# Optimization experiments

Measured on AMD Instinct MI355X. Metric: run time of the kernel, lower is better.

## Reference

```python
import jax, jax.numpy as jnp
import numpy as np

E = 8           # experts (num_experts // world_size, world_size=1)
D = 1024        # hidden_size
H = 4096        # expert FFN hidden = 4*D
CAP_FACTOR = 1.25
LOSS_COEF = 0.01


def setup_inputs() -> dict:
    key = jax.random.key(0)
    k0, k1, k2, k3 = jax.random.split(key, 4)
    B, N = 8, 2048
    x = jax.random.normal(k0, (B, N, D), jnp.float32)
    Wg = jax.random.normal(k1, (D, E), jnp.float32) * (D ** -0.5)
    W1 = jax.random.normal(k2, (E, D, H), jnp.float32) * (D ** -0.5)
    b1 = jnp.zeros((E, H), jnp.float32)
    W2 = jax.random.normal(k3, (E, H, D), jnp.float32) * (H ** -0.5)
    b2 = jnp.zeros((E, D), jnp.float32)
    return {"hidden_states": x, "Wg": Wg, "W1": W1, "b1": b1, "W2": W2, "b2": b2}


def reference(hidden_states, Wg, W1, b1, W2, b2):
    x = hidden_states
    B, N, Dm = x.shape
    S = B * N
    C = int(S * CAP_FACTOR / E)      # shared expert capacity (top1+top2)
    xt = x.reshape(S, Dm)

    # --- top-2 gating ---
    gates = jax.nn.softmax(xt @ Wg, axis=-1)                       # [S, E]
    idx1 = jnp.argmax(gates, axis=-1)                              # [S]
    gate1 = jnp.take_along_axis(gates, idx1[:, None], axis=-1)[:, 0]
    gates_m = gates.at[jnp.arange(S), idx1].set(-1.0)
    idx2 = jnp.argmax(gates_m, axis=-1)
    gate2 = jnp.take_along_axis(gates, idx2[:, None], axis=-1)[:, 0]

    mask1 = jax.nn.one_hot(idx1, E, dtype=xt.dtype)                # [S, E]
    mask2 = jax.nn.one_hot(idx2, E, dtype=xt.dtype)

    # positions within each expert's buffer (top-1 first, then top-2)
    pos1 = jnp.take_along_axis(jnp.cumsum(mask1, axis=0), idx1[:, None], axis=1)[:, 0] - 1.0
    keep1 = (pos1 < C).astype(xt.dtype)
    used1 = jnp.sum(mask1 * keep1[:, None], axis=0)                # [E] slots taken by top-1
    pos2 = jnp.take_along_axis(jnp.cumsum(mask2, axis=0), idx2[:, None], axis=1)[:, 0] - 1.0
    pos2 = pos2 + used1[idx2]
    keep2 = (pos2 < C).astype(xt.dtype)

    # renormalize surviving gates
    denom = gate1 * keep1 + gate2 * keep2 + 1e-9
    g1 = gate1 * keep1 / denom
    g2 = gate2 * keep2 / denom

    p1 = jnp.where(keep1 > 0, pos1, 0.0).astype(jnp.int32)
    p2 = jnp.where(keep2 > 0, pos2, 0.0).astype(jnp.int32)

    # --- dispatch (scatter tokens into [E, C, D] expert buffers) ---
    buf = jnp.zeros((E, C, Dm), xt.dtype)
    buf = buf.at[idx1, p1].add(xt * keep1[:, None])
    buf = buf.at[idx2, p2].add(xt * keep2[:, None])

    # --- expert grouped FFN ---
    h = jax.nn.gelu(jnp.einsum('ecd,edh->ech', buf, W1) + b1[:, None, :])
    eo = jnp.einsum('ech,ehd->ecd', h, W2) + b2[:, None, :]       # [E, C, D]

    # --- combine (gather + weight) ---
    y = g1[:, None] * eo[idx1, p1] + g2[:, None] * eo[idx2, p2]    # [S, D]

    # --- load-balancing aux loss ---
    me = jnp.mean(gates, axis=0)        # density proxy
    ce = jnp.mean(mask1, axis=0)        # actual top-1 density
    loss = LOSS_COEF * jnp.mean(me * ce) * (E * E)

    # output dropout is identity in eval / deterministic mode
    return y.reshape(B, N, Dm), loss
```

## Files before the change

kernel.cpp:

```cpp
#include <hip/hip_runtime.h>
#include <hip/hip_bf16.h>

#define S_TOKENS 16384
#define DMODEL   1024
#define NEXP     8
#define HFF      4096
#define CAP      2560
#define OUT_TOTAL (S_TOKENS * DMODEL + 1)
#define NCHUNK   64

typedef __attribute__((ext_vector_type(8))) short bf16x8;
typedef __attribute__((ext_vector_type(4))) float f32x4;

__device__ inline float bf2f(unsigned short u) {
    union { unsigned int i; float f; } v; v.i = ((unsigned int)u) << 16; return v.f;
}
__device__ inline unsigned short f2bf(float f) {
    __hip_bfloat16 h = __float2bfloat16(f);
    return *reinterpret_cast<unsigned short*>(&h);
}
__device__ inline float ldg(const void* p, size_t i, int f32i) {
    return f32i ? ((const float*)p)[i] : bf2f(((const ushort*)p)[i]);
}
__device__ inline float gelu_tanh(float x) {
    float u = 0.7978845608028654f * (x + 0.044715f * x * x * x);
    return 0.5f * x * (1.0f + tanhf(u));
}
__device__ inline void lds16(const void* g, void* l) {
    __builtin_amdgcn_global_load_lds((const __attribute__((address_space(1))) unsigned int*)g,
                                     (__attribute__((address_space(3))) unsigned int*)l, 16, 0, 0);
}

__global__ void detect_kernel(const ushort* __restrict__ xus, int* __restrict__ flag) {
    const int lane = threadIdx.x;
    int cnt = 0;
#pragma unroll
    for (int j = 0; j < 16; j++) {
        int p = lane * 16 + j;
        int eb = (xus[2 * p] >> 7) & 0xFF;
        cnt += (eb >= 100 && eb <= 140) ? 1 : 0;
    }
#pragma unroll
    for (int off = 32; off > 0; off >>= 1) cnt += __shfl_down(cnt, off, 64);
    if (lane == 0) flag[0] = (cnt < 512) ? 1 : 0;
}

__global__ __launch_bounds__(256) void zero_kernel(void* __restrict__ out, const int* __restrict__ dflag) {
    const int f32i = *dflag;
    for (size_t i = (size_t)blockIdx.x * 256 + threadIdx.x; i < OUT_TOTAL; i += (size_t)gridDim.x * 256) {
        if (f32i) ((float*)out)[i] = 0.f; else ((ushort*)out)[i] = 0;
    }
}

__global__ __launch_bounds__(256) void zeroeo_kernel(float* __restrict__ p, size_t n) {
    for (size_t i = (size_t)blockIdx.x * 256 + threadIdx.x; i < n; i += (size_t)gridDim.x * 256)
        p[i] = 0.f;
}

__global__ __launch_bounds__(256) void convx_kernel(const void* __restrict__ x, const int* __restrict__ dflag,
                                                    ushort* __restrict__ xb) {
    const int f32i = *dflag;
    for (size_t i = (size_t)blockIdx.x * 256 + threadIdx.x; i < (size_t)S_TOKENS * DMODEL;
         i += (size_t)gridDim.x * 256)
        xb[i] = f32i ? f2bf(((const float*)x)[i]) : ((const ushort*)x)[i];
}

__global__ __launch_bounds__(256) void gate_kernel(const void* __restrict__ x, const void* __restrict__ Wg,
                                                   const int* __restrict__ dflag,
                                                   float* __restrict__ gate1, float* __restrict__ gate2,
                                                   int* __restrict__ idx1, int* __restrict__ idx2,
                                                   float* __restrict__ bsum) {
    __shared__ float wgs[DMODEL * NEXP];
    __shared__ float gsh[4][NEXP];
    const int t = threadIdx.x;
    const int f32i = *dflag;
    for (int i = t; i < DMODEL * NEXP; i += 256) wgs[i] = ldg(Wg, i, f32i);
    __syncthreads();
    const int wave = t >> 6, lane = t & 63;
    const int s = blockIdx.x * 4 + wave;
    float acc[NEXP];
#pragma unroll
    for (int e = 0; e < NEXP; e++) acc[e] = 0.f;
#pragma unroll
    for (int i = 0; i < 16; i++) {
        int d = i * 64 + lane;
        float xv = ldg(x, (size_t)s * DMODEL + d, f32i);
        const float* w = &wgs[d * NEXP];
#pragma unroll
        for (int e = 0; e < NEXP; e++) acc[e] += xv * w[e];
    }
#pragma unroll
    for (int off = 32; off > 0; off >>= 1)
#pragma unroll
        for (int e = 0; e < NEXP; e++) acc[e] += __shfl_down(acc[e], off, 64);
    if (lane == 0) {
        float mx = acc[0];
#pragma unroll
        for (int e = 1; e < NEXP; e++) mx = fmaxf(mx, acc[e]);
        float p[NEXP], se = 0.f;
#pragma unroll
        for (int e = 0; e < NEXP; e++) { p[e] = __expf(acc[e] - mx); se += p[e]; }
        float inv = 1.0f / se;
#pragma unroll
        for (int e = 0; e < NEXP; e++) p[e] *= inv;
        int i1 = 0; float g1v = p[0];
#pragma unroll
        for (int e = 1; e < NEXP; e++) if (p[e] > g1v) { g1v = p[e]; i1 = e; }
        int i2 = -1; float g2v = -1.0f;
#pragma unroll
        for (int e = 0; e < NEXP; e++) if (e != i1 && p[e] > g2v) { g2v = p[e]; i2 = e; }
        gate1[s] = g1v; gate2[s] = g2v; idx1[s] = i1; idx2[s] = i2;
#pragma unroll
        for (int e = 0; e < NEXP; e++) gsh[wave][e] = p[e];
    }
    __syncthreads();
    if (t < NEXP) bsum[blockIdx.x * NEXP + t] = gsh[0][t] + gsh[1][t] + gsh[2][t] + gsh[3][t];
}

__global__ __launch_bounds__(256) void hist_kernel(const int* __restrict__ idx1, const int* __restrict__ idx2,
                                                   const float* __restrict__ bsum,
                                                   int* __restrict__ c1, int* __restrict__ c2,
                                                   float* __restrict__ msumB, int* __restrict__ rowmap) {
    const int b = blockIdx.x, t = threadIdx.x;
    const int w = t >> 6, lane = t & 63;
    __shared__ int sc1[4][NEXP], sc2[4][NEXP];
    __shared__ float sm[256];

    for (int i = b * 256 + t; i < NEXP * CAP; i += NCHUNK * 256) rowmap[i] = -1;

    const int s = b * 256 + w * 64 + lane;
    const int id1 = idx1[s], id2 = idx2[s];
#pragma unroll
    for (int e = 0; e < NEXP; e++) {
        unsigned long long m1 = __ballot(id1 == e);
        unsigned long long m2 = __ballot(id2 == e);
        if (lane == 0) { sc1[w][e] = __popcll(m1); sc2[w][e] = __popcll(m2); }
    }
    sm[t] = bsum[b * 512 + t] + bsum[b * 512 + 256 + t];
    __syncthreads();
    if (t < NEXP) {
        c1[b * NEXP + t] = sc1[0][t] + sc1[1][t] + sc1[2][t] + sc1[3][t];
        c2[b * NEXP + t] = sc2[0][t] + sc2[1][t] + sc2[2][t] + sc2[3][t];
        float ms = 0.f;
#pragma unroll
        for (int k = 0; k < 32; k++) ms += sm[t + NEXP * k];
        msumB[b * NEXP + t] = ms;
    }
}

__global__ void base_kernel(const int* __restrict__ c1, const int* __restrict__ c2,
                            const float* __restrict__ msumB, const int* __restrict__ dflag,
                            int* __restrict__ base1, int* __restrict__ base2, void* __restrict__ out) {
    const int lane = threadIdx.x;
    float contrib = 0.f;
    if (lane < NEXP) {
        int run = 0;
        for (int b = 0; b < NCHUNK; b++) { base1[b * NEXP + lane] = run; run += c1[b * NEXP + lane]; }
        const int count1 = run;
        int run2 = count1 < CAP ? count1 : CAP;
        for (int b = 0; b < NCHUNK; b++) { base2[b * NEXP + lane] = run2; run2 += c2[b * NEXP + lane]; }
        float ms = 0.f;
        for (int b = 0; b < NCHUNK; b++) ms += msumB[b * NEXP + lane];
        contrib = (ms / (float)S_TOKENS) * ((float)count1 / (float)S_TOKENS);
    }
#pragma unroll
    for (int off = 4; off > 0; off >>= 1) contrib += __shfl_down(contrib, off, 64);
    if (lane == 0) {
        float L = 0.08f * contrib;
        if (*dflag) ((float*)out)[(size_t)S_TOKENS * DMODEL] = L;
        else        ((ushort*)out)[(size_t)S_TOKENS * DMODEL] = f2bf(L);
    }
}

__global__ __launch_bounds__(256) void place_kernel(const int* __restrict__ idx1, const int* __restrict__ idx2,
                                                    const int* __restrict__ base1, const int* __restrict__ base2,
                                                    int* __restrict__ p1i, int* __restrict__ p2i,
                                                    int* __restrict__ rowmap) {
    const int b = blockIdx.x, t = threadIdx.x;
    const int w = t >> 6, lane = t & 63;
    const unsigned long long below = (1ull << lane) - 1ull;
    __shared__ int wc1[4][NEXP], wc2[4][NEXP];
    const int s = b * 256 + w * 64 + lane;
    const int id1 = idx1[s], id2 = idx2[s];
    int r1 = 0, r2 = 0;
#pragma unroll
    for (int e = 0; e < NEXP; e++) {
        unsigned long long m1 = __ballot(id1 == e);
        if (id1 == e) r1 = __popcll(m1 & below);
        unsigned long long m2 = __ballot(id2 == e);
        if (id2 == e) r2 = __popcll(m2 & below);
        if (lane == 0) { wc1[w][e] = __popcll(m1); wc2[w][e] = __popcll(m2); }
    }
    __syncthreads();
    int off1 = 0, off2 = 0;
#pragma unroll
    for (int ww = 0; ww < 3; ww++) {
        if (ww < w) { off1 += wc1[ww][id1]; off2 += wc2[ww][id2]; }
    }
    const int pos1 = base1[b * NEXP + id1] + off1 + r1;
    if (pos1 < CAP) { p1i[s] = pos1; rowmap[id1 * CAP + pos1] = s; } else p1i[s] = -1;
    const int pos2 = base2[b * NEXP + id2] + off2 + r2;
    if (pos2 < CAP) { p2i[s] = pos2; rowmap[id2 * CAP + pos2] = s; } else p2i[s] = -1;
}

__global__ __launch_bounds__(256) void transpose_conv(const void* __restrict__ src, ushort* __restrict__ dst,
                                                      const int* __restrict__ dflag,
                                                      long srcBase, int srcStride, int dstStride,
                                                      long srcExpStride, long dstExpStride) {
    __shared__ ushort tile[64][68];
    const int f32i = *dflag;
    srcBase += (long)blockIdx.z * srcExpStride;
    dst     += (size_t)blockIdx.z * dstExpStride;
    const int c0 = blockIdx.x * 64, r0 = blockIdx.y * 64;
    const int tx = threadIdx.x & 15, ty = threadIdx.x >> 4;
#pragma unroll
    for (int k = 0; k < 4; k++) {
        int row = ty + 16 * k;
        size_t b = (size_t)srcBase + (size_t)(r0 + row) * srcStride + c0 + tx * 4;
#pragma unroll
        for (int j = 0; j < 4; j++) tile[row][tx * 4 + j] = f2bf(ldg(src, b + j, f32i));
    }
    __syncthreads();
#pragma unroll
    for (int k = 0; k < 4; k++) {
        int orow = ty + 16 * k;
        ushort4 v;
        v.x = tile[tx * 4 + 0][orow];
        v.y = tile[tx * 4 + 1][orow];
        v.z = tile[tx * 4 + 2][orow];
        v.w = tile[tx * 4 + 3][orow];
        *(ushort4*)(dst + (size_t)(c0 + orow) * dstStride + r0 + tx * 4) = v;
    }
}

template<int NC>
__global__ __launch_bounds__(256) void gemm1_kernel(const ushort* __restrict__ xb,
                                                    const int* __restrict__ rowmapBase,
                                                    const ushort* __restrict__ T,
                                                    const void* __restrict__ b1, long biasBase,
                                                    const int* __restrict__ dflag,
                                                    ushort* __restrict__ hout) {
    __shared__ ushort lA[128 * 32];
    __shared__ ushort lB[128 * 32];
    const int z = blockIdx.z;
    const int* rowmapE = rowmapBase + z * CAP;
    T    += (size_t)z * NC * DMODEL;
    hout += (size_t)z * CAP * NC;
    biasBase += (long)z * HFF;
    const int t = threadIdx.x;
    const int w = t >> 6, lane = t & 63;
    const int n0 = blockIdx.x * 128, m0 = blockIdx.y * 128;
    const int wr = w >> 1, wc = w & 1;
    const int l15 = lane & 15, quad = lane >> 4;
    const int swz = (lane >> 3) & 3;
    const int q2 = quad ^ ((l15 >> 1) & 3);

    int arow[2];
#pragma unroll
    for (int it = 0; it < 2; it++) {
        int r = (it * 2048 + w * 512 + lane * 8) >> 5;
        int rm = rowmapE[m0 + r];
        arow[it] = rm < 0 ? 0 : rm;
    }

    f32x4 acc[4][4];
#pragma unroll
    for (int i = 0; i < 4; i++)
#pragma unroll
        for (int j = 0; j < 4; j++) acc[i][j] = (f32x4){0.f, 0.f, 0.f, 0.f};

    for (int k0 = 0; k0 < DMODEL; k0 += 32) {
        __syncthreads();
#pragma unroll
        for (int it = 0; it < 2; it++) {
            int f = it * 2048 + w * 512 + lane * 8;
            int r = f >> 5, kk = (f & 31) ^ (swz << 3);
            lds16(xb + (size_t)arow[it] * DMODEL + k0 + kk, &lA[it * 2048 + w * 512]);
            lds16(T + (size_t)(n0 + r) * DMODEL + k0 + kk, &lB[it * 2048 + w * 512]);
        }
        __syncthreads();
        bf16x8 af[4], bfr[4];
#pragma unroll
        for (int i = 0; i < 4; i++) af[i] = *(const bf16x8*)&lA[(wr * 64 + i * 16 + l15) * 32 + q2 * 8];
#pragma unroll
        for (int j = 0; j < 4; j++) bfr[j] = *(const bf16x8*)&lB[(wc * 64 + j * 16 + l15) * 32 + q2 * 8];
#pragma unroll
        for (int i = 0; i < 4; i++)
#pragma unroll
            for (int j = 0; j < 4; j++)
                acc[i][j] = __builtin_amdgcn_mfma_f32_16x16x32_bf16(af[i], bfr[j], acc[i][j], 0, 0, 0);
    }
    const int f32i = *dflag;
    float bv[4];
#pragma unroll
    for (int j = 0; j < 4; j++) bv[j] = ldg(b1, biasBase + n0 + wc * 64 + j * 16 + l15, f32i);
#pragma unroll
    for (int i = 0; i < 4; i++) {
        int row0 = m0 + wr * 64 + i * 16 + quad * 4;
#pragma unroll
        for (int j = 0; j < 4; j++) {
            int col = n0 + wc * 64 + j * 16 + l15;
#pragma unroll
            for (int r = 0; r < 4; r++)
                hout[(size_t)(row0 + r) * NC + col] = f2bf(gelu_tanh(acc[i][j][r] + bv[j]));
        }
    }
}

template<int KC>
__global__ __launch_bounds__(256) void gemm2f_kernel(const ushort* __restrict__ h,
                                                     const ushort* __restrict__ T2,
                                                     float* __restrict__ eo32) {
    __shared__ ushort lA[128 * 32];
    __shared__ ushort lB[128 * 32];
    const int ze = blockIdx.z;
    h    += (size_t)ze * CAP * KC;
    T2   += (size_t)ze * DMODEL * KC;
    eo32 += (size_t)ze * CAP * DMODEL;
    const int t = threadIdx.x;
    const int w = t >> 6, lane = t & 63;
    const int n0 = blockIdx.x * 128, m0 = blockIdx.y * 128;
    const int wr = w >> 1, wc = w & 1;
    const int l15 = lane & 15, quad = lane >> 4;
    const int swz = (lane >> 3) & 3;
    const int q2 = quad ^ ((l15 >> 1) & 3);

    f32x4 acc[4][4];
#pragma unroll
    for (int i = 0; i < 4; i++)
#pragma unroll
        for (int j = 0; j < 4; j++) acc[i][j] = (f32x4){0.f, 0.f, 0.f, 0.f};

    for (int k0 = 0; k0 < KC; k0 += 32) {
        __syncthreads();
#pragma unroll
        for (int it = 0; it < 2; it++) {
            int f = it * 2048 + w * 512 + lane * 8;
            int r = f >> 5, kk = (f & 31) ^ (swz << 3);
            lds16(h  + (size_t)(m0 + r) * KC + k0 + kk, &lA[it * 2048 + w * 512]);
            lds16(T2 + (size_t)(n0 + r) * KC + k0 + kk, &lB[it * 2048 + w * 512]);
        }
        __syncthreads();
        bf16x8 af[4], bfr[4];
#pragma unroll
        for (int i = 0; i < 4; i++) af[i] = *(const bf16x8*)&lA[(wr * 64 + i * 16 + l15) * 32 + q2 * 8];
#pragma unroll
        for (int j = 0; j < 4; j++) bfr[j] = *(const bf16x8*)&lB[(wc * 64 + j * 16 + l15) * 32 + q2 * 8];
#pragma unroll
        for (int i = 0; i < 4; i++)
#pragma unroll
            for (int j = 0; j < 4; j++)
                acc[i][j] = __builtin_amdgcn_mfma_f32_16x16x32_bf16(af[i], bfr[j], acc[i][j], 0, 0, 0);
    }
#pragma unroll
    for (int i = 0; i < 4; i++) {
#pragma unroll
        for (int r = 0; r < 4; r++) {
            int row = m0 + wr * 64 + i * 16 + quad * 4 + r;
#pragma unroll
            for (int j = 0; j < 4; j++) {
                int col = n0 + wc * 64 + j * 16 + l15;
                eo32[(size_t)row * DMODEL + col] = acc[i][j][r];
            }
        }
    }
}

template<int KC, int KB>
__global__ __launch_bounds__(256) void gemm2s_kernel(const ushort* __restrict__ h,
                                                     const ushort* __restrict__ T2,
                                                     float* __restrict__ eo32) {
    __shared__ ushort lA[128 * 32];
    __shared__ ushort lB[128 * 32];
    constexpr int KSPLIT = KC / KB;
    const int zz = blockIdx.z;
    const int ze = zz / KSPLIT, zk = zz - ze * KSPLIT;
    h    += (size_t)ze * CAP * KC;
    T2   += (size_t)ze * DMODEL * KC;
    eo32 += (size_t)ze * CAP * DMODEL;
    const int t = threadIdx.x;
    const int w = t >> 6, lane = t & 63;
    const int n0 = blockIdx.x * 128, m0 = blockIdx.y * 128;
    const int kbeg = zk * KB;
    const int wr = w >> 1, wc = w & 1;
    const int l15 = lane & 15, quad = lane >> 4;
    const int swz = (lane >> 3) & 3;
    const int q2 = quad ^ ((l15 >> 1) & 3);

    f32x4 acc[4][4];
#pragma unroll
    for (int i = 0; i < 4; i++)
#pragma unroll
        for (int j = 0; j < 4; j++) acc[i][j] = (f32x4){0.f, 0.f, 0.f, 0.f};

    for (int k0 = kbeg; k0 < kbeg + KB; k0 += 32) {
        __syncthreads();
#pragma unroll
        for (int it = 0; it < 2; it++) {
            int f = it * 2048 + w * 512 + lane * 8;
            int r = f >> 5, kk = (f & 31) ^ (swz << 3);
            lds16(h  + (size_t)(m0 + r) * KC + k0 + kk, &lA[it * 2048 + w * 512]);
            lds16(T2 + (size_t)(n0 + r) * KC + k0 + kk, &lB[it * 2048 + w * 512]);
        }
        __syncthreads();
        bf16x8 af[4], bfr[4];
#pragma unroll
        for (int i = 0; i < 4; i++) af[i] = *(const bf16x8*)&lA[(wr * 64 + i * 16 + l15) * 32 + q2 * 8];
#pragma unroll
        for (int j = 0; j < 4; j++) bfr[j] = *(const bf16x8*)&lB[(wc * 64 + j * 16 + l15) * 32 + q2 * 8];
#pragma unroll
        for (int i = 0; i < 4; i++)
#pragma unroll
            for (int j = 0; j < 4; j++)
                acc[i][j] = __builtin_amdgcn_mfma_f32_16x16x32_bf16(af[i], bfr[j], acc[i][j], 0, 0, 0);
    }
#pragma unroll
    for (int i = 0; i < 4; i++) {
#pragma unroll
        for (int r = 0; r < 4; r++) {
            int row = m0 + wr * 64 + i * 16 + quad * 4 + r;
#pragma unroll
            for (int j = 0; j < 4; j++) {
                int col = n0 + wc * 64 + j * 16 + l15;
                atomicAdd(&eo32[(size_t)row * DMODEL + col], acc[i][j][r]);
            }
        }
    }
}

__global__ __launch_bounds__(256) void combine_kernel(const float* __restrict__ eo32, const void* __restrict__ b2,
                                                      long b2Base, const int* __restrict__ dflag,
                                                      const int* __restrict__ rowmapE, const int* __restrict__ idx1,
                                                      const int* __restrict__ p1i, const int* __restrict__ p2i,
                                                      const float* __restrict__ gate1, const float* __restrict__ gate2,
                                                      int expert, void* __restrict__ out) {
    const int t = threadIdx.x;
    const int f32i = *dflag;
    const int c0 = t * 4;
    float bv[4];
#pragma unroll
    for (int j = 0; j < 4; j++) bv[j] = ldg(b2, b2Base + c0 + j, f32i);
    for (int r = blockIdx.x; r < CAP; r += gridDim.x) {
        int s = rowmapE[r];
        if (s < 0) continue;
        float g1 = gate1[s], g2 = gate2[s];
        float k1 = (p1i[s] >= 0) ? 1.f : 0.f, k2 = (p2i[s] >= 0) ? 1.f : 0.f;
        float denom = g1 * k1 + g2 * k2 + 1e-9f;
        float wgt = ((idx1[s] == expert) ? g1 : g2) / denom;
        float4 ev = *(const float4*)&eo32[(size_t)r * DMODEL + c0];
        size_t oi = (size_t)s * DMODEL + c0;
        if (f32i) {
            float4* po = (float4*)((float*)out + oi);
            float4 ov = *po;
            ov.x += wgt * (ev.x + bv[0]); ov.y += wgt * (ev.y + bv[1]);
            ov.z += wgt * (ev.z + bv[2]); ov.w += wgt * (ev.w + bv[3]);
            *po = ov;
        } else {
            ushort* po = (ushort*)out + oi;
            ushort4 ov = *(ushort4*)po;
            ov.x = f2bf(bf2f(ov.x) + wgt * (ev.x + bv[0]));
            ov.y = f2bf(bf2f(ov.y) + wgt * (ev.y + bv[1]));
            ov.z = f2bf(bf2f(ov.z) + wgt * (ev.z + bv[2]));
            ov.w = f2bf(bf2f(ov.w) + wgt * (ev.w + bv[3]));
            *(ushort4*)po = ov;
        }
    }
}

__global__ __launch_bounds__(256) void combine_all_kernel(const float* __restrict__ eoall,
                                                          const void* __restrict__ b2,
                                                          const int* __restrict__ dflag,
                                                          const int* __restrict__ idx1, const int* __restrict__ idx2,
                                                          const int* __restrict__ p1i, const int* __restrict__ p2i,
                                                          const float* __restrict__ gate1, const float* __restrict__ gate2,
                                                          void* __restrict__ out) {
    const int s = blockIdx.x;
    const int t = threadIdx.x;
    const int c0 = t * 4;
    const int f32i = *dflag;
    const int e1 = idx1[s], e2 = idx2[s];
    const int p1 = p1i[s], p2 = p2i[s];
    const float g1 = gate1[s], g2 = gate2[s];
    const float k1 = (p1 >= 0) ? 1.f : 0.f, k2 = (p2 >= 0) ? 1.f : 0.f;
    const float denom = g1 * k1 + g2 * k2 + 1e-9f;
    const float w1 = g1 * k1 / denom, w2 = g2 * k2 / denom;
    float r0 = 0.f, r1 = 0.f, r2 = 0.f, r3 = 0.f;
    if (p1 >= 0) {
        const float4 ev = *(const float4*)&eoall[((size_t)e1 * CAP + p1) * DMODEL + c0];
        long bb = (long)e1 * DMODEL + c0;
        r0 += w1 * (ev.x + ldg(b2, bb + 0, f32i));
        r1 += w1 * (ev.y + ldg(b2, bb + 1, f32i));
        r2 += w1 * (ev.z + ldg(b2, bb + 2, f32i));
        r3 += w1 * (ev.w + ldg(b2, bb + 3, f32i));
    }
    if (p2 >= 0) {
        const float4 ev = *(const float4*)&eoall[((size_t)e2 * CAP + p2) * DMODEL + c0];
        long bb = (long)e2 * DMODEL + c0;
        r0 += w2 * (ev.x + ldg(b2, bb + 0, f32i));
        r1 += w2 * (ev.y + ldg(b2, bb + 1, f32i));
        r2 += w2 * (ev.z + ldg(b2, bb + 2, f32i));
        r3 += w2 * (ev.w + ldg(b2, bb + 3, f32i));
    }
    size_t oi = (size_t)s * DMODEL + c0;
    if (f32i) {
        float4 ov; ov.x = r0; ov.y = r1; ov.z = r2; ov.w = r3;
        *(float4*)((float*)out + oi) = ov;
    } else {
        ushort4 ov; ov.x = f2bf(r0); ov.y = f2bf(r1); ov.z = f2bf(r2); ov.w = f2bf(r3);
        *(ushort4*)((ushort*)out + oi) = ov;
    }
}

struct WsPtrs {
    int *flag, *rowmap, *idx1, *idx2, *p1i, *p2i, *c1, *c2, *base1, *base2;
    float *gate1, *gate2, *bsum, *msumB;
    ushort* xb;
};
static WsPtrs ws_ptrs(char* ws) {
    WsPtrs p;
    p.flag   = (int*)ws;
    p.rowmap = (int*)(ws + 256);
    p.gate1  = (float*)(ws + 82176);
    p.gate2  = (float*)(ws + 147712);
    p.idx1   = (int*)(ws + 213248);
    p.idx2   = (int*)(ws + 278784);
    p.p1i    = (int*)(ws + 344320);
    p.p2i    = (int*)(ws + 409856);
    p.bsum   = (float*)(ws + 475392);
    p.c1     = (int*)(ws + 606464);
    p.c2     = (int*)(ws + 608512);
    p.msumB  = (float*)(ws + 610560);
    p.base1  = (int*)(ws + 612608);
    p.base2  = (int*)(ws + 614656);
    p.xb     = (ushort*)(ws + 655360);
    return p;
}
static void prologue(const void* x, const void* Wg, const WsPtrs& p, void* out, hipStream_t stream,
                     bool zeroOut) {
    detect_kernel<<<dim3(1), 64, 0, stream>>>((const ushort*)x, p.flag);
    if (zeroOut) zero_kernel<<<dim3(16384), 256, 0, stream>>>(out, p.flag);
    convx_kernel<<<dim3(8192), 256, 0, stream>>>(x, p.flag, p.xb);
    gate_kernel<<<dim3(S_TOKENS / 4), 256, 0, stream>>>(x, Wg, p.flag, p.gate1, p.gate2, p.idx1, p.idx2, p.bsum);
    hist_kernel<<<dim3(NCHUNK), 256, 0, stream>>>(p.idx1, p.idx2, p.bsum, p.c1, p.c2, p.msumB, p.rowmap);
    base_kernel<<<dim3(1), 64, 0, stream>>>(p.c1, p.c2, p.msumB, p.flag, p.base1, p.base2, out);
    place_kernel<<<dim3(NCHUNK), 256, 0, stream>>>(p.idx1, p.idx2, p.base1, p.base2, p.p1i, p.p2i, p.rowmap);
}

template<int EB>
static void run_moe_batched(const void* x, const void* Wg, const void* W1, const void* b1,
                            const void* W2, const void* b2, void* out, char* ws, hipStream_t stream,
                            bool fullCombine) {
    WsPtrs p = ws_ptrs(ws);
    char* cur = ws + 655360 + 33554432;
    ushort* h = (ushort*)cur;  cur += (size_t)EB * CAP * HFF * 2;
    ushort* T = (ushort*)cur;  cur += (size_t)EB * HFF * DMODEL * 2;
    float* eo = (float*)cur;

    prologue(x, Wg, p, out, stream, !fullCombine);
    for (int b = 0; b < NEXP / EB; b++) {
        const int e0 = b * EB;
        float* eoS = fullCombine ? eo + (size_t)e0 * CAP * DMODEL : eo;
        transpose_conv<<<dim3(HFF / 64, DMODEL / 64, EB), 256, 0, stream>>>(
            W1, T, p.flag, (long)e0 * DMODEL * HFF, HFF, DMODEL,
            (long)DMODEL * HFF, (long)HFF * DMODEL);
        gemm1_kernel<HFF><<<dim3(HFF / 128, CAP / 128, EB), 256, 0, stream>>>(
            p.xb, p.rowmap + e0 * CAP, T, b1, (long)e0 * HFF, p.flag, h);
        transpose_conv<<<dim3(DMODEL / 64, HFF / 64, EB), 256, 0, stream>>>(
            W2, T, p.flag, (long)e0 * HFF * DMODEL, DMODEL, HFF,
            (long)HFF * DMODEL, (long)DMODEL * HFF);
        if (fullCombine) {
            gemm2f_kernel<HFF><<<dim3(DMODEL / 128, CAP / 128, EB), 256, 0, stream>>>(h, T, eoS);
        } else {
            zeroeo_kernel<<<dim3(4096), 256, 0, stream>>>(eoS, (size_t)EB * CAP * DMODEL);
            gemm2s_kernel<HFF, 1024><<<dim3(DMODEL / 128, CAP / 128, 4 * EB), 256, 0, stream>>>(h, T, eoS);
            for (int q = 0; q < EB; q++)
                combine_kernel<<<dim3(1280), 256, 0, stream>>>(
                    eo + (size_t)q * CAP * DMODEL, b2, (long)(e0 + q) * DMODEL, p.flag,
                    p.rowmap + (e0 + q) * CAP, p.idx1, p.p1i, p.p2i, p.gate1, p.gate2, e0 + q, out);
        }
    }
    if (fullCombine)
        combine_all_kernel<<<dim3(S_TOKENS), 256, 0, stream>>>(
            eo, b2, p.flag, p.idx1, p.idx2, p.p1i, p.p2i, p.gate1, p.gate2, out);
}

static void run_moe_a(const void* x, const void* Wg, const void* W1, const void* b1,
                      const void* W2, const void* b2, void* out, char* ws, hipStream_t stream) {
    WsPtrs p = ws_ptrs(ws);
    ushort* h    = (ushort*)(ws + 655360 + 33554432);
    ushort* T    = (ushort*)(ws + 655360 + 33554432 + 20971520);
    float*  eo32 = (float*)(ws + 655360 + 33554432 + 20971520 + 8388608);

    prologue(x, Wg, p, out, stream, true);
    for (int e = 0; e < NEXP; e++) {
        transpose_conv<<<dim3(HFF / 64, DMODEL / 64), 256, 0, stream>>>(
            W1, T, p.flag, (long)e * DMODEL * HFF, HFF, DMODEL, 0, 0);
        gemm1_kernel<HFF><<<dim3(HFF / 128, CAP / 128), 256, 0, stream>>>(
            p.xb, p.rowmap + e * CAP, T, b1, (long)e * HFF, p.flag, h);
        zeroeo_kernel<<<dim3(2048), 256, 0, stream>>>(eo32, (size_t)CAP * DMODEL);
        transpose_conv<<<dim3(DMODEL / 64, HFF / 64), 256, 0, stream>>>(
            W2, T, p.flag, (long)e * HFF * DMODEL, DMODEL, HFF, 0, 0);
        gemm2s_kernel<HFF, 512><<<dim3(DMODEL / 128, CAP / 128, HFF / 512), 256, 0, stream>>>(h, T, eo32);
        combine_kernel<<<dim3(1280), 256, 0, stream>>>(
            eo32, b2, (long)e * DMODEL, p.flag, p.rowmap + e * CAP,
            p.idx1, p.p1i, p.p2i, p.gate1, p.gate2, e, out);
    }
}

static void run_moe_b(const void* x, const void* Wg, const void* W1, const void* b1,
                      const void* W2, const void* b2, void* out, char* ws, hipStream_t stream) {
    WsPtrs p = ws_ptrs(ws);
    const int HC = 2048;
    ushort* h    = (ushort*)(ws + 655360 + 33554432);
    ushort* T    = (ushort*)(ws + 655360 + 33554432 + 10485760);
    float*  eo32 = (float*)(ws + 655360 + 33554432 + 10485760 + 4194304);

    prologue(x, Wg, p, out, stream, true);
    for (int e = 0; e < NEXP; e++) {
        zeroeo_kernel<<<dim3(2048), 256, 0, stream>>>(eo32, (size_t)CAP * DMODEL);
        for (int c = 0; c < HFF / HC; c++) {
            const long hoff = (long)c * HC;
            transpose_conv<<<dim3(HC / 64, DMODEL / 64), 256, 0, stream>>>(
                W1, T, p.flag, (long)e * DMODEL * HFF + hoff, HFF, DMODEL, 0, 0);
            gemm1_kernel<HC><<<dim3(HC / 128, CAP / 128), 256, 0, stream>>>(
                p.xb, p.rowmap + e * CAP, T, b1, (long)e * HFF + hoff, p.flag, h);
            transpose_conv<<<dim3(DMODEL / 64, HC / 64), 256, 0, stream>>>(
                W2, T, p.flag, (long)e * HFF * DMODEL + hoff * DMODEL, DMODEL, HC, 0, 0);
            gemm2s_kernel<2048, 1024><<<dim3(DMODEL / 128, CAP / 128, 2), 256, 0, stream>>>(h, T, eo32);
        }
        combine_kernel<<<dim3(1280), 256, 0, stream>>>(
            eo32, b2, (long)e * DMODEL, p.flag, p.rowmap + e * CAP,
            p.idx1, p.p1i, p.p2i, p.gate1, p.gate2, e, out);
    }
}

extern "C" void kernel_launch(void* const* d_in, const int* in_sizes, int n_in,
                              void* d_out, int out_size, void* d_ws, size_t ws_size,
                              hipStream_t stream) {
    const void* x  = d_in[0];
    const void* Wg = d_in[1];
    const void* W1 = d_in[2];
    const void* b1 = d_in[3];
    const void* W2 = d_in[4];
    const void* b2 = d_in[5];
    char* ws = (char*)d_ws;

    if (ws_size >= 239500000ull)      run_moe_batched<4>(x, Wg, W1, b1, W2, b2, d_out, ws, stream, true);
    else if (ws_size >= 181000000ull) run_moe_batched<2>(x, Wg, W1, b1, W2, b2, d_out, ws, stream, true);
    else if (ws_size >= 118000000ull) run_moe_batched<2>(x, Wg, W1, b1, W2, b2, d_out, ws, stream, false);
    else if (ws_size >= 78000000ull)  run_moe_a(x, Wg, W1, b1, W2, b2, d_out, ws, stream);
    else                              run_moe_b(x, Wg, W1, b1, W2, b2, d_out, ws, stream);
}
```

Measured before the change: 1.142 ms.

## Remap GEMM blocks per XCD for L2 locality and use 8-wave gemm2 tiles

Both GEMM kernels now take a flattened 1D grid and remap block IDs so that consecutive blocks sent round-robin to the 8 XCDs each work on a contiguous chunk of tiles. The aim is better L2 reuse of the A and B tiles within each XCD. The full-combine gemm2 kernel also moves to 512 threads, with 8 waves each computing 64x32 of the 128x128 tile. This halves the per-thread accumulators and loads each LDS tile with a single 16-byte load per thread, at the cost of more waves per block competing for LDS and sync barriers.

Result: faster. 1.002 ms (-12.2%).

```diff
diff --git a/kernel.cpp b/kernel.cpp
--- a/kernel.cpp
+++ b/kernel.cpp
@@ -233,7 +233,7 @@
     }
 }
 
-template<int NC>
+template<int NC, int EB>
 __global__ __launch_bounds__(256) void gemm1_kernel(const ushort* __restrict__ xb,
                                                     const int* __restrict__ rowmapBase,
                                                     const ushort* __restrict__ T,
@@ -242,14 +242,19 @@
                                                     ushort* __restrict__ hout) {
     __shared__ ushort lA[128 * 32];
     __shared__ ushort lB[128 * 32];
-    const int z = blockIdx.z;
+    constexpr int TN = NC / 128, TM = CAP / 128;
+    constexpr int TOTAL = TN * TM * EB, CHUNK = TOTAL / 8;
+    const int l = blockIdx.x;
+    const int ord = (l & 7) * CHUNK + (l >> 3);
+    const int z = ord / (TN * TM);
+    const int rem = ord - z * (TN * TM);
+    const int m0 = (rem / TN) * 128, n0 = (rem % TN) * 128;
     const int* rowmapE = rowmapBase + z * CAP;
     T    += (size_t)z * NC * DMODEL;
     hout += (size_t)z * CAP * NC;
     biasBase += (long)z * HFF;
     const int t = threadIdx.x;
     const int w = t >> 6, lane = t & 63;
-    const int n0 = blockIdx.x * 128, m0 = blockIdx.y * 128;
     const int wr = w >> 1, wc = w & 1;
     const int l15 = lane & 15, quad = lane >> 4;
     const int swz = (lane >> 3) & 3;
@@ -307,49 +312,50 @@
     }
 }
 
-template<int KC>
-__global__ __launch_bounds__(256) void gemm2f_kernel(const ushort* __restrict__ h,
-                                                     const ushort* __restrict__ T2,
-                                                     float* __restrict__ eo32) {
+template<int KC, int EB>
+__global__ __launch_bounds__(512) void gemm2f8_kernel(const ushort* __restrict__ h,
+                                                      const ushort* __restrict__ T2,
+                                                      float* __restrict__ eo32) {
     __shared__ ushort lA[128 * 32];
     __shared__ ushort lB[128 * 32];
-    const int ze = blockIdx.z;
+    constexpr int TN = DMODEL / 128, TM = CAP / 128;
+    constexpr int TOTAL = TN * TM * EB, CHUNK = TOTAL / 8;
+    const int l = blockIdx.x;
+    const int ord = (l & 7) * CHUNK + (l >> 3);
+    const int ze = ord / (TN * TM);
+    const int rem = ord - ze * (TN * TM);
+    const int m0 = (rem / TN) * 128, n0 = (rem % TN) * 128;
     h    += (size_t)ze * CAP * KC;
     T2   += (size_t)ze * DMODEL * KC;
     eo32 += (size_t)ze * CAP * DMODEL;
     const int t = threadIdx.x;
     const int w = t >> 6, lane = t & 63;
-    const int n0 = blockIdx.x * 128, m0 = blockIdx.y * 128;
-    const int wr = w >> 1, wc = w & 1;
+    const int wr = w >> 2, wc = w & 3;
     const int l15 = lane & 15, quad = lane >> 4;
-    const int swz = (lane >> 3) & 3;
     const int q2 = quad ^ ((l15 >> 1) & 3);
-
-    f32x4 acc[4][4];
+    const int sr = t >> 2;
+    const int kk = ((t & 3) * 8) ^ (((t >> 3) & 3) << 3);
+
+    f32x4 acc[4][2];
 #pragma unroll
     for (int i = 0; i < 4; i++)
 #pragma unroll
-        for (int j = 0; j < 4; j++) acc[i][j] = (f32x4){0.f, 0.f, 0.f, 0.f};
+        for (int j = 0; j < 2; j++) acc[i][j] = (f32x4){0.f, 0.f, 0.f, 0.f};
 
     for (int k0 = 0; k0 < KC; k0 += 32) {
         __syncthreads();
-#pragma unroll
-        for (int it = 0; it < 2; it++) {
-            int f = it * 2048 + w * 512 + lane * 8;
-            int r = f >> 5, kk = (f & 31) ^ (swz << 3);
-            lds16(h  + (size_t)(m0 + r) * KC + k0 + kk, &lA[it * 2048 + w * 512]);
-            lds16(T2 + (size_t)(n0 + r) * KC + k0 + kk, &lB[it * 2048 + w * 512]);
-        }
+        lds16(h  + (size_t)(m0 + sr) * KC + k0 + kk, &lA[t * 8]);
+        lds16(T2 + (size_t)(n0 + sr) * KC + k0 + kk, &lB[t * 8]);
         __syncthreads();
-        bf16x8 af[4], bfr[4];
+        bf16x8 af[4], bfr[2];
 #pragma unroll
         for (int i = 0; i < 4; i++) af[i] = *(const bf16x8*)&lA[(wr * 64 + i * 16 + l15) * 32 + q2 * 8];
 #pragma unroll
-        for (int j = 0; j < 4; j++) bfr[j] = *(const bf16x8*)&lB[(wc * 64 + j * 16 + l15) * 32 + q2 * 8];
+        for (int j = 0; j < 2; j++) bfr[j] = *(const bf16x8*)&lB[(wc * 32 + j * 16 + l15) * 32 + q2 * 8];
 #pragma unroll
         for (int i = 0; i < 4; i++)
 #pragma unroll
-            for (int j = 0; j < 4; j++)
+            for (int j = 0; j < 2; j++)
                 acc[i][j] = __builtin_amdgcn_mfma_f32_16x16x32_bf16(af[i], bfr[j], acc[i][j], 0, 0, 0);
     }
 #pragma unroll
@@ -358,8 +364,8 @@
         for (int r = 0; r < 4; r++) {
             int row = m0 + wr * 64 + i * 16 + quad * 4 + r;
 #pragma unroll
-            for (int j = 0; j < 4; j++) {
-                int col = n0 + wc * 64 + j * 16 + l15;
+            for (int j = 0; j < 2; j++) {
+                int col = n0 + wc * 32 + j * 16 + l15;
                 eo32[(size_t)row * DMODEL + col] = acc[i][j][r];
             }
         }
@@ -563,13 +569,13 @@
         transpose_conv<<<dim3(HFF / 64, DMODEL / 64, EB), 256, 0, stream>>>(
             W1, T, p.flag, (long)e0 * DMODEL * HFF, HFF, DMODEL,
             (long)DMODEL * HFF, (long)HFF * DMODEL);
-        gemm1_kernel<HFF><<<dim3(HFF / 128, CAP / 128, EB), 256, 0, stream>>>(
+        gemm1_kernel<HFF, EB><<<dim3((HFF / 128) * (CAP / 128) * EB), 256, 0, stream>>>(
             p.xb, p.rowmap + e0 * CAP, T, b1, (long)e0 * HFF, p.flag, h);
         transpose_conv<<<dim3(DMODEL / 64, HFF / 64, EB), 256, 0, stream>>>(
             W2, T, p.flag, (long)e0 * HFF * DMODEL, DMODEL, HFF,
             (long)HFF * DMODEL, (long)DMODEL * HFF);
         if (fullCombine) {
-            gemm2f_kernel<HFF><<<dim3(DMODEL / 128, CAP / 128, EB), 256, 0, stream>>>(h, T, eoS);
+            gemm2f8_kernel<HFF, EB><<<dim3((DMODEL / 128) * (CAP / 128) * EB), 512, 0, stream>>>(h, T, eoS);
         } else {
             zeroeo_kernel<<<dim3(4096), 256, 0, stream>>>(eoS, (size_t)EB * CAP * DMODEL);
             gemm2s_kernel<HFF, 1024><<<dim3(DMODEL / 128, CAP / 128, 4 * EB), 256, 0, stream>>>(h, T, eoS);
@@ -595,7 +601,7 @@
     for (int e = 0; e < NEXP; e++) {
         transpose_conv<<<dim3(HFF / 64, DMODEL / 64), 256, 0, stream>>>(
             W1, T, p.flag, (long)e * DMODEL * HFF, HFF, DMODEL, 0, 0);
-        gemm1_kernel<HFF><<<dim3(HFF / 128, CAP / 128), 256, 0, stream>>>(
+        gemm1_kernel<HFF, 1><<<dim3((HFF / 128) * (CAP / 128)), 256, 0, stream>>>(
             p.xb, p.rowmap + e * CAP, T, b1, (long)e * HFF, p.flag, h);
         zeroeo_kernel<<<dim3(2048), 256, 0, stream>>>(eo32, (size_t)CAP * DMODEL);
         transpose_conv<<<dim3(DMODEL / 64, HFF / 64), 256, 0, stream>>>(
@@ -622,7 +628,7 @@
             const long hoff = (long)c * HC;
             transpose_conv<<<dim3(HC / 64, DMODEL / 64), 256, 0, stream>>>(
                 W1, T, p.flag, (long)e * DMODEL * HFF + hoff, HFF, DMODEL, 0, 0);
-            gemm1_kernel<HC><<<dim3(HC / 128, CAP / 128), 256, 0, stream>>>(
+            gemm1_kernel<2048, 1><<<dim3((2048 / 128) * (CAP / 128)), 256, 0, stream>>>(
                 p.xb, p.rowmap + e * CAP, T, b1, (long)e * HFF + hoff, p.flag, h);
             transpose_conv<<<dim3(DMODEL / 64, HC / 64), 256, 0, stream>>>(
                 W2, T, p.flag, (long)e * HFF * DMODEL + hoff * DMODEL, DMODEL, HC, 0, 0);
```
